# Performance work log

Hardware: AMD Instinct MI355X
Metric: run time of the kernel (lower is better)

Reference implementation:

```python
import jax, jax.numpy as jnp
import numpy as np

B, U, L, H, M = 4, 16, 128, 768, 256   # docs, utterances/doc, tokens/utt, hidden, mentions/doc
HID = 150                               # Score MLP hidden dim
N_CLUSTERS = 32


def setup_inputs() -> dict:
    key = jax.random.key(0)
    ks = jax.random.split(key, 8)
    hidden = jax.random.normal(ks[0], (B, U, L, H), jnp.float32)

    rng = np.random.default_rng(0)
    span_utt = rng.integers(0, U, (B, M))
    span_start = rng.integers(0, L - 8, (B, M))
    span_end = span_start + rng.integers(1, 9, (B, M))  # span length in [1, 8]

    # coreference labels: label[i, j] = 1 iff j is a true antecedent (j < i, same cluster);
    # if mention i has no antecedent, label[i, i] = 1 (the epsilon / new-entity slot).
    clusters = rng.integers(0, N_CLUSTERS, (B, M))
    same = clusters[:, :, None] == clusters[:, None, :]
    ant = same & np.tril(np.ones((M, M), bool), -1)
    labels = ant.astype(np.float32)
    diag = np.arange(M)
    labels[:, diag, diag] = (~ant.any(-1)).astype(np.float32)

    scale = 0.02
    W1 = jax.random.normal(ks[1], (3 * H, HID), jnp.float32) * scale
    W2 = jax.random.normal(ks[2], (HID, HID), jnp.float32) * scale
    W3 = jax.random.normal(ks[3], (HID, 1), jnp.float32) * scale
    return {
        "hidden": hidden,
        "span_utt": jnp.asarray(span_utt, jnp.int32),
        "span_start": jnp.asarray(span_start, jnp.int32),
        "span_end": jnp.asarray(span_end, jnp.int32),
        "labels": jnp.asarray(labels),
        "W1": W1, "b1": jnp.zeros((HID,), jnp.float32),
        "W2": W2, "b2": jnp.zeros((HID,), jnp.float32),
        "W3": W3, "b3": jnp.zeros((1,), jnp.float32),
    }


def reference(hidden, span_utt, span_start, span_end, labels, W1, b1, W2, b2, W3, b3):
    # ---- span mean-pooling (EntityEncoder, aggr='mean') ----
    pos = jnp.arange(L)
    mask = (pos[None, None, :] >= span_start[..., None]) & (pos[None, None, :] < span_end[..., None])
    w = mask.astype(hidden.dtype) / (span_end - span_start)[..., None].astype(hidden.dtype)  # [B,M,L]
    gathered = jnp.take_along_axis(hidden, span_utt[:, :, None, None], axis=1)  # [B,M,L,H]
    pooled = jnp.einsum('bml,bmlh->bmh', w, gathered)  # [B,M,H]

    # ---- pairwise antecedent scoring (PairScorer / Score MLP, dropout=eval) ----
    ii, jj = np.tril_indices(M, -1)  # static pair indices, P = M(M-1)/2
    # concat(i_g, j_g, i_g*j_g) @ W1  ==  i_g@W1a + j_g@W1b + (i_g*j_g)@W1c
    W1a, W1b, W1c = W1[:H], W1[H:2 * H], W1[2 * H:]
    hi = pooled @ W1a   # [B,M,HID]
    hj = pooled @ W1b   # [B,M,HID]
    prod = pooled[:, ii] * pooled[:, jj]                    # [B,P,H]
    h1 = jax.nn.relu(hi[:, ii] + hj[:, jj] + prod @ W1c + b1)
    h2 = jax.nn.relu(h1 @ W2 + b2)
    s = (h2 @ W3 + b3)[..., 0]  # [B,P]

    # ---- per-mention ragged softmax, padded to [M, M] with -1000 ----
    # row i has logits s_ij for j<i plus epsilon=0 at j=i (diagonal of zeros matrix)
    logits = jnp.zeros((B, M, M), hidden.dtype).at[:, ii, jj].set(s)
    valid = jnp.tril(jnp.ones((M, M), bool))
    probs = jax.nn.softmax(jnp.where(valid, logits, -1e30), axis=-1)
    probs = jnp.where(valid, probs, jnp.asarray(-1000.0, hidden.dtype))

    # ---- compute_loss ----
    eps = 1e-8
    prob_sum = jnp.sum(jnp.clip(probs * labels, eps, 1.0 - eps), axis=-1)  # [B,M]
    loss = -jnp.sum(jnp.log(prob_sum))
    return loss
```

## Files before the change

kernel.cpp:

```cpp
#include <hip/hip_runtime.h>
#include <hip/hip_bf16.h>

#define B_ 4
#define U_ 16
#define L_ 128
#define H_ 768
#define M_ 256
#define HID_ 150

typedef _Float16 half8 __attribute__((ext_vector_type(8)));
typedef _Float16 half4t __attribute__((ext_vector_type(4)));
typedef float floatx4 __attribute__((ext_vector_type(4)));
typedef float floatx16 __attribute__((ext_vector_type(16)));

__device__ __forceinline__ void gl_lds16(const _Float16* g, _Float16* l)
{
    __builtin_amdgcn_global_load_lds(
        (const __attribute__((address_space(1))) unsigned int*)g,
        (__attribute__((address_space(3))) unsigned int*)l, 16, 0, 0);
}

__global__ __launch_bounds__(256) void prep_kernel(
    const float* __restrict__ W1, const float* __restrict__ W2,
    const float* __restrict__ b2, const float* __restrict__ W3,
    _Float16* __restrict__ W1cs, _Float16* __restrict__ W2s,
    _Float16* __restrict__ W1abs, float2* __restrict__ bw)
{
    int idx = blockIdx.x * 256 + threadIdx.x;
    if (blockIdx.x == 0 && threadIdx.x < 160) {
        int n = threadIdx.x;
        bw[n] = (n < HID_) ? make_float2(b2[n], W3[n]) : make_float2(0.f, 0.f);
    }
    if (idx < 122880) {
        int k = idx / 160, n = idx - k * 160;
        float v = (n < HID_) ? W1[(size_t)(2 * H_ + k) * HID_ + n] : 0.f;
        W1cs[(k >> 4) * 2560 + (n >> 5) * 512 +
             (((n & 31) | (((k >> 3) & 1) << 5)) << 3) + (k & 7)] = (_Float16)v;
        return;
    }
    idx -= 122880;
    if (idx < 25600) {
        int k = idx / 160, n = idx - k * 160;
        float v = (k < HID_ && n < HID_) ? W2[(size_t)k * HID_ + n] : 0.f;
        W2s[(k >> 4) * 2560 + (n >> 5) * 512 +
            (((n & 31) | (((k >> 3) & 1) << 5)) << 3) + (k & 7)] = (_Float16)v;
        return;
    }
    idx -= 25600;
    if (idx < 245760) {
        int k = idx / 320, n = idx - k * 320;
        float v = 0.f;
        if (n < HID_) v = W1[(size_t)k * HID_ + n];
        else if (n >= 160 && n < 160 + HID_) v = W1[(size_t)(H_ + k) * HID_ + (n - 160)];
        W1abs[(k >> 5) * 10240 + (n >> 4) * 512 +
              (((n & 15) | (((k >> 3) & 3) << 4)) << 3) + (k & 7)] = (_Float16)v;
    }
}

__global__ __launch_bounds__(256) void pool_kernel(
    const float* __restrict__ hidden, const int* __restrict__ sutt,
    const int* __restrict__ sstart, const int* __restrict__ send,
    _Float16* __restrict__ pooledh)
{
    const int bm = blockIdx.x * 4 + (threadIdx.x >> 6);
    const int lane = threadIdx.x & 63;
    const int b  = bm >> 8;
    const int u  = sutt[bm];
    const int st = sstart[bm];
    const int en = send[bm];
    const float inv = 1.0f / (float)(en - st);
    const float* src = hidden + ((size_t)(b * U_ + u) * L_) * H_ + lane * 12;
    float4 s[3];
    #pragma unroll
    for (int q = 0; q < 3; ++q) s[q] = make_float4(0.f, 0.f, 0.f, 0.f);
    for (int l = st; l < en; ++l) {
        const float* p = src + (size_t)l * H_;
        #pragma unroll
        for (int q = 0; q < 3; ++q) {
            float4 v = *(const float4*)(p + q * 4);
            s[q].x += v.x; s[q].y += v.y; s[q].z += v.z; s[q].w += v.w;
        }
    }
    _Float16* gp = pooledh + (size_t)bm * H_ + lane * 12;
    #pragma unroll
    for (int q = 0; q < 3; ++q) {
        half4t hv;
        hv[0] = (_Float16)(s[q].x * inv); hv[1] = (_Float16)(s[q].y * inv);
        hv[2] = (_Float16)(s[q].z * inv); hv[3] = (_Float16)(s[q].w * inv);
        *(half4t*)(gp + q * 4) = hv;
    }
}

__global__ __launch_bounds__(256) void hihj_kernel(
    const _Float16* __restrict__ pooledh, const float* __restrict__ b1,
    const _Float16* __restrict__ W1abs,
    float* __restrict__ hiF, float* __restrict__ hjT)
{
    __shared__ __align__(16) _Float16 spool[16 * 776];
    const int blk = blockIdx.x;
    const int tid = threadIdx.x;
    for (int e = tid; e < 16 * 96; e += 256) {
        int r = e / 96, c = e - r * 96;
        *(half8*)&spool[r * 776 + c * 8] =
            *(const half8*)&pooledh[(size_t)(blk * 16 + r) * H_ + c * 8];
    }
    __syncthreads();

    const int w = tid >> 6, lane = tid & 63;
    const int g = lane >> 4, l15 = lane & 15;
    floatx4 acc[5];
    #pragma unroll
    for (int u5 = 0; u5 < 5; ++u5) acc[u5] = (floatx4){0.f, 0.f, 0.f, 0.f};
    const _Float16* aB = &spool[l15 * 776 + g * 8];
    for (int kc = 0; kc < 24; ++kc) {
        half8 av = *(const half8*)(aB + kc * 32);
        #pragma unroll
        for (int u5 = 0; u5 < 5; ++u5) {
            const int u = w * 5 + u5;
            half8 bv = *(const half8*)(W1abs + (size_t)((kc * 20 + u) * 64 + lane) * 8);
            acc[u5] = __builtin_amdgcn_mfma_f32_16x16x32_f16(av, bv, acc[u5], 0, 0, 0);
        }
    }
    const int row0 = blk * 16 + g * 4;
    #pragma unroll
    for (int u5 = 0; u5 < 5; ++u5) {
        const int n = (w * 5 + u5) * 16 + l15;
        if (n < HID_) {
            float b1v = b1[n];
            #pragma unroll
            for (int r = 0; r < 4; ++r)
                hiF[(size_t)(row0 + r) * 160 + n] = acc[u5][r] + b1v;
        } else if (n >= 160 && n < 160 + HID_) {
            *(float4*)&hjT[(size_t)(n - 160) * 1024 + row0] =
                make_float4(acc[u5][0], acc[u5][1], acc[u5][2], acc[u5][3]);
        }
    }
}

__global__ __launch_bounds__(128, 2) void pair_mlp_kernel(
    const _Float16* __restrict__ pooledh,
    const float* __restrict__ hiF, const float* __restrict__ hjT,
    const _Float16* __restrict__ W1cs, const _Float16* __restrict__ W2s,
    const float2* __restrict__ bw, const float* __restrict__ b3,
    float* __restrict__ logits)
{
    __shared__ __align__(16) _Float16 smem[2 * 5440];

    int q = blockIdx.x;
    const int b = q / 576;
    int r = q - b * 576;
    int jt = 0;
    while (r >= 128 - 16 * jt) { r -= 128 - 16 * jt; ++jt; }
    const int p = 16 * jt + r;
    const int i0 = 2 * p, j0 = jt * 32;
    const int bm = b * M_;
    const int w = threadIdx.x >> 6;
    const int lane = threadIdx.x & 63;
    const int c31 = lane & 31;
    const int hw = lane >> 5;

    _Float16* Wb0 = smem;
    _Float16* Wb1 = smem + 5120;
    _Float16* h1w = smem + w * 5440;

    const _Float16* pjp = pooledh + (size_t)(bm + j0 + c31) * H_ + (hw << 3);
    const _Float16* pip = pooledh + (size_t)(bm + i0 + w) * H_ + (hw << 3);

    floatx16 acc1[5];
    #pragma unroll
    for (int t1 = 0; t1 < 5; ++t1)
        #pragma unroll
        for (int e = 0; e < 16; ++e) acc1[t1][e] = 0.f;

    {
        const _Float16* gW = W1cs + (size_t)(5 * w) * 512 + lane * 8;
        #pragma unroll
        for (int c = 0; c < 5; ++c)
            gl_lds16(gW + c * 512, Wb0 + (5 * w + c) * 512);
    }
    half8 Apj0 = *(const half8*)(pjp);
    half8 Apj1 = *(const half8*)(pjp + 16);
    half8 Ai0  = *(const half8*)(pip);
    half8 Ai1  = *(const half8*)(pip + 16);
    __syncthreads();

    for (int kc = 0; kc < 24; ++kc) {
        const _Float16* Wcur = (kc & 1) ? Wb1 : Wb0;
        _Float16*       Wnxt = (kc & 1) ? Wb0 : Wb1;
        half8 npj0, npj1, ni0, ni1;
        if (kc < 23) {
            const _Float16* gW = W1cs + (size_t)(kc + 1) * 5120 + (5 * w) * 512 + lane * 8;
            #pragma unroll
            for (int c = 0; c < 5; ++c)
                gl_lds16(gW + c * 512, Wnxt + (5 * w + c) * 512);
            const int kb = (kc + 1) * 32;
            npj0 = *(const half8*)(pjp + kb);
            npj1 = *(const half8*)(pjp + kb + 16);
            ni0  = *(const half8*)(pip + kb);
            ni1  = *(const half8*)(pip + kb + 16);
        }
        {
            half8 a = Ai0 * Apj0;
            #pragma unroll
            for (int t1 = 0; t1 < 5; ++t1) {
                half8 wf = *(const half8*)&Wcur[t1 * 512 + lane * 8];
                acc1[t1] = __builtin_amdgcn_mfma_f32_32x32x16_f16(wf, a, acc1[t1], 0, 0, 0);
            }
        }
        {
            half8 a = Ai1 * Apj1;
            #pragma unroll
            for (int t1 = 0; t1 < 5; ++t1) {
                half8 wf = *(const half8*)&Wcur[(5 + t1) * 512 + lane * 8];
                acc1[t1] = __builtin_amdgcn_mfma_f32_32x32x16_f16(wf, a, acc1[t1], 0, 0, 0);
            }
        }
        if (kc < 23) { Apj0 = npj0; Apj1 = npj1; Ai0 = ni0; Ai1 = ni1; }
        __syncthreads();
    }

    const int jcol = bm + j0 + c31;
    #pragma unroll
    for (int t1 = 0; t1 < 5; ++t1) {
        #pragma unroll
        for (int qd = 0; qd < 4; ++qd) {
            const int n1 = t1 * 32 + 8 * qd + 4 * hw;
            float hj0 = hjT[(size_t)(n1 + 0) * 1024 + jcol];
            float hj1 = hjT[(size_t)(n1 + 1) * 1024 + jcol];
            float hj2 = hjT[(size_t)(n1 + 2) * 1024 + jcol];
            float hj3 = hjT[(size_t)(n1 + 3) * 1024 + jcol];
            float4 hiv = *(const float4*)&hiF[(size_t)(bm + i0 + w) * 160 + n1];
            half4t hv;
            hv[0] = (_Float16)fmaxf(acc1[t1][4 * qd + 0] + hiv.x + hj0, 0.f);
            hv[1] = (_Float16)fmaxf(acc1[t1][4 * qd + 1] + hiv.y + hj1, 0.f);
            hv[2] = (_Float16)fmaxf(acc1[t1][4 * qd + 2] + hiv.z + hj2, 0.f);
            hv[3] = (_Float16)fmaxf(acc1[t1][4 * qd + 3] + hiv.w + hj3, 0.f);
            *(half4t*)&h1w[c31 * 170 + n1] = hv;
        }
    }
    __syncthreads();

    const float b3v = b3[0];
    floatx16 acc2[5];
    #pragma unroll
    for (int t2 = 0; t2 < 5; ++t2)
        #pragma unroll
        for (int e = 0; e < 16; ++e) acc2[t2][e] = 0.f;

    half8 W2b[2][5], h1b[2];
    #pragma unroll
    for (int c = 0; c < 2; ++c) {
        const _Float16* wb = W2s + (size_t)(c * 5) * 512 + lane * 8;
        #pragma unroll
        for (int t2 = 0; t2 < 5; ++t2) W2b[c][t2] = *(const half8*)(wb + t2 * 512);
        h1b[c] = *(const half8*)&h1w[c31 * 170 + c * 16 + hw * 8];
    }
    for (int kc2 = 0; kc2 < 10; ++kc2) {
        const int cur = kc2 & 1;
        half8 nw[5], nh;
        if (kc2 < 8) {
            const _Float16* wb = W2s + (size_t)((kc2 + 2) * 5) * 512 + lane * 8;
            #pragma unroll
            for (int t2 = 0; t2 < 5; ++t2) nw[t2] = *(const half8*)(wb + t2 * 512);
            nh = *(const half8*)&h1w[c31 * 170 + (kc2 + 2) * 16 + hw * 8];
        }
        #pragma unroll
        for (int t2 = 0; t2 < 5; ++t2)
            acc2[t2] = __builtin_amdgcn_mfma_f32_32x32x16_f16(
                W2b[cur][t2], h1b[cur], acc2[t2], 0, 0, 0);
        if (kc2 < 8) {
            #pragma unroll
            for (int t2 = 0; t2 < 5; ++t2) W2b[cur][t2] = nw[t2];
            h1b[cur] = nh;
        }
    }

    float sown = 0.f;
    #pragma unroll
    for (int t2 = 0; t2 < 5; ++t2) {
        #pragma unroll
        for (int qd = 0; qd < 4; ++qd) {
            const int n2 = t2 * 32 + 8 * qd + 4 * hw;
            float4 bw01 = *(const float4*)&bw[n2];
            float4 bw23 = *(const float4*)&bw[n2 + 2];
            sown += fmaxf(acc2[t2][4 * qd + 0] + bw01.x, 0.f) * bw01.y;
            sown += fmaxf(acc2[t2][4 * qd + 1] + bw01.z, 0.f) * bw01.w;
            sown += fmaxf(acc2[t2][4 * qd + 2] + bw23.x, 0.f) * bw23.y;
            sown += fmaxf(acc2[t2][4 * qd + 3] + bw23.z, 0.f) * bw23.w;
        }
    }
    float s = sown + __shfl_xor(sown, 32);
    const int i = i0 + w;
    const int j = j0 + c31;
    if (lane < 32 && j < i)
        logits[(size_t)(bm + i) * M_ + j] = s + b3v;
}

__global__ __launch_bounds__(256) void loss_kernel(
    const float* __restrict__ logits, const float* __restrict__ labels,
    float* __restrict__ out)
{
    const int bm = blockIdx.x;
    const int i  = bm & (M_ - 1);
    const int j  = threadIdx.x;
    __shared__ float red[4];
    __shared__ float bcast;

    float val = (j < i) ? logits[(size_t)bm * M_ + j]
                        : ((j == i) ? 0.0f : -1e30f);

    float m = val;
    #pragma unroll
    for (int off = 32; off >= 1; off >>= 1) m = fmaxf(m, __shfl_down(m, off, 64));
    const int wave = j >> 6, lane = j & 63;
    if (lane == 0) red[wave] = m;
    __syncthreads();
    if (j == 0) bcast = fmaxf(fmaxf(red[0], red[1]), fmaxf(red[2], red[3]));
    __syncthreads();
    const float mm = bcast;

    float e = (j <= i) ? expf(val - mm) : 0.0f;
    float s = e;
    #pragma unroll
    for (int off = 32; off >= 1; off >>= 1) s += __shfl_down(s, off, 64);
    __syncthreads();
    if (lane == 0) red[wave] = s;
    __syncthreads();
    if (j == 0) bcast = red[0] + red[1] + red[2] + red[3];
    __syncthreads();
    const float ssum = bcast;

    float prob = (j <= i) ? (e / ssum) : -1000.0f;
    float lab = labels[(size_t)bm * M_ + j];
    float tv = prob * lab;
    tv = fminf(fmaxf(tv, 1e-8f), 1.0f - 1e-8f);
    float rs = tv;
    #pragma unroll
    for (int off = 32; off >= 1; off >>= 1) rs += __shfl_down(rs, off, 64);
    __syncthreads();
    if (lane == 0) red[wave] = rs;
    __syncthreads();
    if (j == 0) atomicAdd(out, -logf(red[0] + red[1] + red[2] + red[3]));
}

extern "C" void kernel_launch(void* const* d_in, const int* in_sizes, int n_in,
                              void* d_out, int out_size, void* d_ws, size_t ws_size,
                              hipStream_t stream)
{
    const float* hidden = (const float*)d_in[0];
    const int*   sutt   = (const int*)d_in[1];
    const int*   sstart = (const int*)d_in[2];
    const int*   send   = (const int*)d_in[3];
    const float* labels = (const float*)d_in[4];
    const float* W1     = (const float*)d_in[5];
    const float* b1     = (const float*)d_in[6];
    const float* W2     = (const float*)d_in[7];
    const float* b2     = (const float*)d_in[8];
    const float* W3     = (const float*)d_in[9];
    const float* b3     = (const float*)d_in[10];

    float* ws = (float*)d_ws;
    float*    hiF     = ws;
    float*    hjT     = ws + 163840;
    float*    logits  = ws + 327680;
    float2*   bw      = (float2*)(ws + 589824);
    _Float16* pooledh = (_Float16*)(ws + 590144);
    _Float16* W1cs    = (_Float16*)(ws + 983360);
    _Float16* W2s     = (_Float16*)(ws + 1106240);
    _Float16* W1abs   = (_Float16*)(ws + 1119040);
    float* out = (float*)d_out;

    hipMemsetAsync(d_out, 0, sizeof(float), stream);

    prep_kernel<<<dim3(1540), 256, 0, stream>>>(W1, W2, b2, W3,
                                                W1cs, W2s, W1abs, bw);
    pool_kernel<<<dim3(256), 256, 0, stream>>>(hidden, sutt, sstart, send, pooledh);
    hihj_kernel<<<dim3(64), 256, 0, stream>>>(pooledh, b1, W1abs, hiF, hjT);
    pair_mlp_kernel<<<dim3(576 * B_), 128, 0, stream>>>(pooledh, hiF, hjT,
                                                        W1cs, W2s, bw, b3, logits);
    loss_kernel<<<dim3(B_ * M_), 256, 0, stream>>>(logits, labels, out);
}
```

Before: 202.2 us.

## Triple-buffer W1c loads with partial vmcnt waits and fuse prep with pooling

The pair MLP's first GEMM loop moves from a double-buffered LDS ring with a full __syncthreads each step to a three-slot ring. The weight chunk is prefetched two iterations ahead, and each step waits only on the older loads via explicit s_waitcnt vmcnt before a raw s_barrier, so global-to-LDS latency overlaps more MFMA work. Separately, the weight-prep and span-pooling kernels are merged into one launch with disjoint block ranges, removing one kernel launch and letting the two independent jobs run concurrently. The hand-written vmcnt counts depend on how the compiler orders memory operations and could break correctness if that order changes, and the LDS footprint grows slightly.

```diff
diff --git a/kernel.cpp b/kernel.cpp
--- a/kernel.cpp
+++ b/kernel.cpp
@@ -20,12 +20,45 @@
         (__attribute__((address_space(3))) unsigned int*)l, 16, 0, 0);
 }
 
-__global__ __launch_bounds__(256) void prep_kernel(
+__global__ __launch_bounds__(256) void prep_pool_kernel(
     const float* __restrict__ W1, const float* __restrict__ W2,
     const float* __restrict__ b2, const float* __restrict__ W3,
+    const float* __restrict__ hidden, const int* __restrict__ sutt,
+    const int* __restrict__ sstart, const int* __restrict__ send,
     _Float16* __restrict__ W1cs, _Float16* __restrict__ W2s,
-    _Float16* __restrict__ W1abs, float2* __restrict__ bw)
-{
+    _Float16* __restrict__ W1abs, float2* __restrict__ bw,
+    _Float16* __restrict__ pooledh)
+{
+    if (blockIdx.x >= 1540) {
+        const int bm = (blockIdx.x - 1540) * 4 + (threadIdx.x >> 6);
+        const int lane = threadIdx.x & 63;
+        const int b  = bm >> 8;
+        const int u  = sutt[bm];
+        const int st = sstart[bm];
+        const int en = send[bm];
+        const float inv = 1.0f / (float)(en - st);
+        const float* src = hidden + ((size_t)(b * U_ + u) * L_) * H_ + lane * 12;
+        float4 s[3];
+        #pragma unroll
+        for (int q = 0; q < 3; ++q) s[q] = make_float4(0.f, 0.f, 0.f, 0.f);
+        for (int l = st; l < en; ++l) {
+            const float* p = src + (size_t)l * H_;
+            #pragma unroll
+            for (int q = 0; q < 3; ++q) {
+                float4 v = *(const float4*)(p + q * 4);
+                s[q].x += v.x; s[q].y += v.y; s[q].z += v.z; s[q].w += v.w;
+            }
+        }
+        _Float16* gp = pooledh + (size_t)bm * H_ + lane * 12;
+        #pragma unroll
+        for (int q = 0; q < 3; ++q) {
+            half4t hv;
+            hv[0] = (_Float16)(s[q].x * inv); hv[1] = (_Float16)(s[q].y * inv);
+            hv[2] = (_Float16)(s[q].z * inv); hv[3] = (_Float16)(s[q].w * inv);
+            *(half4t*)(gp + q * 4) = hv;
+        }
+        return;
+    }
     int idx = blockIdx.x * 256 + threadIdx.x;
     if (blockIdx.x == 0 && threadIdx.x < 160) {
         int n = threadIdx.x;
@@ -57,40 +90,6 @@
     }
 }
 
-__global__ __launch_bounds__(256) void pool_kernel(
-    const float* __restrict__ hidden, const int* __restrict__ sutt,
-    const int* __restrict__ sstart, const int* __restrict__ send,
-    _Float16* __restrict__ pooledh)
-{
-    const int bm = blockIdx.x * 4 + (threadIdx.x >> 6);
-    const int lane = threadIdx.x & 63;
-    const int b  = bm >> 8;
-    const int u  = sutt[bm];
-    const int st = sstart[bm];
-    const int en = send[bm];
-    const float inv = 1.0f / (float)(en - st);
-    const float* src = hidden + ((size_t)(b * U_ + u) * L_) * H_ + lane * 12;
-    float4 s[3];
-    #pragma unroll
-    for (int q = 0; q < 3; ++q) s[q] = make_float4(0.f, 0.f, 0.f, 0.f);
-    for (int l = st; l < en; ++l) {
-        const float* p = src + (size_t)l * H_;
-        #pragma unroll
-        for (int q = 0; q < 3; ++q) {
-            float4 v = *(const float4*)(p + q * 4);
-            s[q].x += v.x; s[q].y += v.y; s[q].z += v.z; s[q].w += v.w;
-        }
-    }
-    _Float16* gp = pooledh + (size_t)bm * H_ + lane * 12;
-    #pragma unroll
-    for (int q = 0; q < 3; ++q) {
-        half4t hv;
-        hv[0] = (_Float16)(s[q].x * inv); hv[1] = (_Float16)(s[q].y * inv);
-        hv[2] = (_Float16)(s[q].z * inv); hv[3] = (_Float16)(s[q].w * inv);
-        *(half4t*)(gp + q * 4) = hv;
-    }
-}
-
 __global__ __launch_bounds__(256) void hihj_kernel(
     const _Float16* __restrict__ pooledh, const float* __restrict__ b1,
     const _Float16* __restrict__ W1abs,
@@ -144,7 +143,7 @@
     const float2* __restrict__ bw, const float* __restrict__ b3,
     float* __restrict__ logits)
 {
-    __shared__ __align__(16) _Float16 smem[2 * 5440];
+    __shared__ __align__(16) _Float16 smem[3 * 5120];
 
     int q = blockIdx.x;
     const int b = q / 576;
@@ -159,8 +158,6 @@
     const int c31 = lane & 31;
     const int hw = lane >> 5;
 
-    _Float16* Wb0 = smem;
-    _Float16* Wb1 = smem + 5120;
     _Float16* h1w = smem + w * 5440;
 
     const _Float16* pjp = pooledh + (size_t)(bm + j0 + c31) * H_ + (hw << 3);
@@ -176,31 +173,41 @@
         const _Float16* gW = W1cs + (size_t)(5 * w) * 512 + lane * 8;
         #pragma unroll
         for (int c = 0; c < 5; ++c)
-            gl_lds16(gW + c * 512, Wb0 + (5 * w + c) * 512);
-    }
-    half8 Apj0 = *(const half8*)(pjp);
-    half8 Apj1 = *(const half8*)(pjp + 16);
-    half8 Ai0  = *(const half8*)(pip);
-    half8 Ai1  = *(const half8*)(pip + 16);
-    __syncthreads();
-
+            gl_lds16(gW + c * 512, smem + (5 * w + c) * 512);
+        #pragma unroll
+        for (int c = 0; c < 5; ++c)
+            gl_lds16(gW + 5120 + c * 512, smem + 5120 + (5 * w + c) * 512);
+    }
+    half8 Apj0[2], Apj1[2], Ai0[2], Ai1[2];
+    Apj0[0] = *(const half8*)(pjp);
+    Apj1[0] = *(const half8*)(pjp + 16);
+    Ai0[0]  = *(const half8*)(pip);
+    Ai1[0]  = *(const half8*)(pip + 16);
+    asm volatile("s_waitcnt vmcnt(11)" ::: "memory");
+    __builtin_amdgcn_s_barrier();
+    __builtin_amdgcn_sched_barrier(0);
+
+    #pragma unroll
     for (int kc = 0; kc < 24; ++kc) {
-        const _Float16* Wcur = (kc & 1) ? Wb1 : Wb0;
-        _Float16*       Wnxt = (kc & 1) ? Wb0 : Wb1;
-        half8 npj0, npj1, ni0, ni1;
+        const int cur = kc & 1, nxt = (kc + 1) & 1;
+        const _Float16* Wcur = smem + (kc % 3) * 5120;
         if (kc < 23) {
-            const _Float16* gW = W1cs + (size_t)(kc + 1) * 5120 + (5 * w) * 512 + lane * 8;
+            const int kb = (kc + 1) * 32;
+            Apj0[nxt] = *(const half8*)(pjp + kb);
+            Apj1[nxt] = *(const half8*)(pjp + kb + 16);
+            Ai0[nxt]  = *(const half8*)(pip + kb);
+            Ai1[nxt]  = *(const half8*)(pip + kb + 16);
+        }
+        if (kc < 22) {
+            const _Float16* gW = W1cs + (size_t)(kc + 2) * 5120
+                                 + (5 * w) * 512 + lane * 8;
+            _Float16* Wd = smem + ((kc + 2) % 3) * 5120;
             #pragma unroll
             for (int c = 0; c < 5; ++c)
-                gl_lds16(gW + c * 512, Wnxt + (5 * w + c) * 512);
-            const int kb = (kc + 1) * 32;
-            npj0 = *(const half8*)(pjp + kb);
-            npj1 = *(const half8*)(pjp + kb + 16);
-            ni0  = *(const half8*)(pip + kb);
-            ni1  = *(const half8*)(pip + kb + 16);
+                gl_lds16(gW + c * 512, Wd + (5 * w + c) * 512);
         }
         {
-            half8 a = Ai0 * Apj0;
+            half8 a = Ai0[cur] * Apj0[cur];
             #pragma unroll
             for (int t1 = 0; t1 < 5; ++t1) {
                 half8 wf = *(const half8*)&Wcur[t1 * 512 + lane * 8];
@@ -208,16 +215,21 @@
             }
         }
         {
-            half8 a = Ai1 * Apj1;
+            half8 a = Ai1[cur] * Apj1[cur];
             #pragma unroll
             for (int t1 = 0; t1 < 5; ++t1) {
                 half8 wf = *(const half8*)&Wcur[(5 + t1) * 512 + lane * 8];
                 acc1[t1] = __builtin_amdgcn_mfma_f32_32x32x16_f16(wf, a, acc1[t1], 0, 0, 0);
             }
         }
-        if (kc < 23) { Apj0 = npj0; Apj1 = npj1; Ai0 = ni0; Ai1 = ni1; }
-        __syncthreads();
-    }
+        if (kc < 22)       asm volatile("s_waitcnt vmcnt(11)" ::: "memory");
+        else if (kc == 22) asm volatile("s_waitcnt vmcnt(6)" ::: "memory");
+        if (kc < 23) {
+            __builtin_amdgcn_s_barrier();
+            __builtin_amdgcn_sched_barrier(0);
+        }
+    }
+    __syncthreads();
 
     const int jcol = bm + j0 + c31;
     #pragma unroll
@@ -372,9 +384,9 @@
 
     hipMemsetAsync(d_out, 0, sizeof(float), stream);
 
-    prep_kernel<<<dim3(1540), 256, 0, stream>>>(W1, W2, b2, W3,
-                                                W1cs, W2s, W1abs, bw);
-    pool_kernel<<<dim3(256), 256, 0, stream>>>(hidden, sutt, sstart, send, pooledh);
+    prep_pool_kernel<<<dim3(1796), 256, 0, stream>>>(
+        W1, W2, b2, W3, hidden, sutt, sstart, send,
+        W1cs, W2s, W1abs, bw, pooledh);
     hihj_kernel<<<dim3(64), 256, 0, stream>>>(pooledh, b1, W1abs, hiF, hjT);
     pair_mlp_kernel<<<dim3(576 * B_), 128, 0, stream>>>(pooledh, hiF, hjT,
                                                         W1cs, W2s, bw, b3, logits);
```

New measurement: 196.2 us. 1.03x faster.
